# Performance work log

Hardware: AMD Instinct MI355X
Metric: run time of the kernel (lower is better)

## Reference

```python
import jax, jax.numpy as jnp
import numpy as np

B, S_ENC, S_DEC = 4, 2048, 1024
ENC_DIM, DEC_DIM, H = 1024, 1024, 16
CROSS_DIM = max(ENC_DIM, DEC_DIM)
HEAD_DIM_DEC = DEC_DIM // H
SCALE = HEAD_DIM_DEC ** 0.5  # module divides by dec_scaling only


def _linear_params(key, d_in, d_out):
    kw, kb = jax.random.split(key)
    bound = 1.0 / np.sqrt(d_in)
    W = jax.random.uniform(kw, (d_in, d_out), jnp.float32, -bound, bound)
    b = jax.random.uniform(kb, (d_out,), jnp.float32, -bound, bound)
    return W, b


def setup_inputs() -> dict:
    key = jax.random.key(0)
    ks = jax.random.split(key, 7)
    enc = jax.random.normal(ks[0], (B, S_ENC, ENC_DIM), jnp.float32)
    dec = jax.random.normal(ks[1], (B, S_DEC, DEC_DIM), jnp.float32)
    enc_mask = jax.random.uniform(ks[2], (B, 1, 1, S_ENC)) < 0.1
    q_w, q_b = _linear_params(ks[3], DEC_DIM, CROSS_DIM)
    k_w, k_b = _linear_params(ks[4], ENC_DIM, CROSS_DIM)
    v_w, v_b = _linear_params(ks[5], ENC_DIM, DEC_DIM)
    o_w, o_b = _linear_params(ks[6], DEC_DIM, DEC_DIM)
    return {"enc": enc, "enc_mask": enc_mask, "dec": dec,
            "q_w": q_w, "q_b": q_b, "k_w": k_w, "k_b": k_b,
            "v_w": v_w, "v_b": v_b, "o_w": o_w, "o_b": o_b}


def _split_heads(x):
    b, s, d = x.shape
    return x.reshape(b, s, H, d // H).transpose(0, 2, 1, 3)  # [b,h,s,hd]


def reference(enc, enc_mask, dec, q_w, q_b, k_w, k_b, v_w, v_b, o_w, o_b):
    q = _split_heads(dec @ q_w + q_b)   # [B,H,Sq,cross_hd]
    k = _split_heads(enc @ k_w + k_b)   # [B,H,Sk,cross_hd]
    v = _split_heads(enc @ v_w + v_b)   # [B,H,Sk,dec_hd]
    logits = jnp.einsum('bhqd,bhkd->bhqk', q, k) / SCALE
    logits = jnp.where(enc_mask, -jnp.inf, logits)
    a = jax.nn.softmax(logits, axis=-1)
    x = jnp.einsum('bhqk,bhkd->bhqd', a, v)          # [B,H,Sq,dec_hd]
    x = x.transpose(0, 2, 1, 3).reshape(x.shape[0], x.shape[2], -1)  # [B,Sq,DEC_DIM]
    return x @ o_w + o_b
```

## Files before the change

kernel.cpp:

```cpp
#include <hip/hip_runtime.h>
#include <hip/hip_bf16.h>
#include <cstdint>

#define BB   4
#define SENC 2048
#define SDEC 1024
#define DM   1024
#define NH   16
#define HD   64

using short8 = __attribute__((ext_vector_type(8))) short;
using f32x4  = __attribute__((ext_vector_type(4))) float;

__device__ inline unsigned short f2bf(float f) {
    return (unsigned short)((__builtin_bit_cast(unsigned int, f) + 0x8000u) >> 16);
}
__device__ inline unsigned int pk2bf(float a, float b) {
    return ((__builtin_bit_cast(unsigned int, a) + 0x8000u) >> 16) |
           ((__builtin_bit_cast(unsigned int, b) + 0x8000u) & 0xffff0000u);
}

__device__ inline float fexp2(float x) {
#if __has_builtin(__builtin_amdgcn_exp2f)
    return __builtin_amdgcn_exp2f(x);
#else
    return exp2f(x);
#endif
}

#if __has_builtin(__builtin_amdgcn_global_load_lds)
#define HAS_GLL 1
#endif

__device__ inline void stage16(const void* g, void* l) {
#ifdef HAS_GLL
    typedef __attribute__((address_space(1))) const unsigned int guint;
    typedef __attribute__((address_space(3))) unsigned int luint;
    __builtin_amdgcn_global_load_lds((guint*)g, (luint*)l, 16, 0, 0);
#else
    *(short8*)l = *(const short8*)g;
#endif
}

__global__ __launch_bounds__(256) void cvt2_kernel(const float* __restrict__ dec,
                                                   const float* __restrict__ enc,
                                                   unsigned short* __restrict__ out) {
    const int nd = BB * SDEC * DM;
    int i = (blockIdx.x * 256 + threadIdx.x) * 4;
    const float* src = (i < nd) ? (dec + i) : (enc + (i - nd));
    float4 v = *(const float4*)src;
    ushort4 o;
    o.x = f2bf(v.x); o.y = f2bf(v.y); o.z = f2bf(v.z); o.w = f2bf(v.w);
    *(ushort4*)(out + i) = o;
}

__global__ __launch_bounds__(256) void wtrans_kernel(
    const float* __restrict__ qw, const float* __restrict__ kw,
    const float* __restrict__ vw, const float* __restrict__ ow,
    unsigned short* __restrict__ qwt, unsigned short* __restrict__ kvwt,
    unsigned short* __restrict__ owt) {
    const float* src; unsigned short* dst;
    switch (blockIdx.z) {
        case 0:  src = qw; dst = qwt; break;
        case 1:  src = kw; dst = kvwt; break;
        case 2:  src = vw; dst = kvwt + (size_t)1024 * DM; break;
        default: src = ow; dst = owt; break;
    }
    __shared__ float t[64][65];
    const int k0 = blockIdx.y * 64, n0 = blockIdx.x * 64;
    const int tid = threadIdx.x;
    #pragma unroll
    for (int it = 0; it < 16; ++it) {
        int e = it * 256 + tid, r = e >> 6, c = e & 63;
        t[r][c] = src[(size_t)(k0 + r) * DM + n0 + c];
    }
    __syncthreads();
    #pragma unroll
    for (int it = 0; it < 16; ++it) {
        int e = it * 256 + tid, r = e >> 6, c = e & 63;
        dst[(size_t)(n0 + r) * DM + k0 + c] = f2bf(t[c][r]);
    }
}

__global__ __launch_bounds__(256) void gemm_qkv_kernel(
    const unsigned short* __restrict__ encb, const unsigned short* __restrict__ decb,
    const unsigned short* __restrict__ kvwt, const unsigned short* __restrict__ qwt,
    const float* __restrict__ q_b, const float* __restrict__ k_b, const float* __restrict__ v_b,
    unsigned short* __restrict__ Qb, unsigned short* __restrict__ Kb,
    unsigned short* __restrict__ Vtb) {
    __shared__ __align__(16) unsigned short As[2][128 * 32];
    __shared__ __align__(16) unsigned short Bs[2][128 * 32];
    const int id = blockIdx.x;
    const bool isKV = id < 1024;
    const unsigned short *A, *Bt;
    int m0, n0;
    if (isKV) {
        const int x = id & 7, w = id >> 3;
        A = encb; Bt = kvwt;
        m0 = (x * 8 + (w >> 4)) * 128;
        n0 = (w & 15) * 128;
    } else {
        const int i2 = id - 1024, x = i2 & 7, w = i2 >> 3;
        A = decb; Bt = qwt;
        m0 = (x * 4 + (w >> 3)) * 128;
        n0 = (w & 7) * 128;
    }
    const int tid = threadIdx.x;
    const int wave = tid >> 6, lane = tid & 63, quad = lane >> 4, l16 = lane & 15;
    const int wr = wave >> 1, wc = wave & 1;
    const int r16 = lane >> 2, c8 = (lane & 3) * 8;
    f32x4 acc[4][4] = {};

    #pragma unroll
    for (int i = 0; i < 2; ++i) {
        const int row = wave * 32 + i * 16 + r16;
        stage16(&A[(size_t)(m0 + row) * DM + c8], &As[0][row * 32 + c8]);
        stage16(&Bt[(size_t)(n0 + row) * DM + c8], &Bs[0][row * 32 + c8]);
    }
    for (int it = 0; it < 32; ++it) {
        const int bf = it & 1;
        __syncthreads();
        if (it < 31) {
            const int kb2 = (it + 1) * 32, nb = bf ^ 1;
            #pragma unroll
            for (int i = 0; i < 2; ++i) {
                const int row = wave * 32 + i * 16 + r16;
                stage16(&A[(size_t)(m0 + row) * DM + kb2 + c8], &As[nb][row * 32 + c8]);
                stage16(&Bt[(size_t)(n0 + row) * DM + kb2 + c8], &Bs[nb][row * 32 + c8]);
            }
        }
        short8 af[4], bfr[4];
        #pragma unroll
        for (int i = 0; i < 4; ++i) af[i] = *(const short8*)&As[bf][(wr * 64 + i * 16 + l16) * 32 + quad * 8];
        #pragma unroll
        for (int j = 0; j < 4; ++j) bfr[j] = *(const short8*)&Bs[bf][(wc * 64 + j * 16 + l16) * 32 + quad * 8];
        #pragma unroll
        for (int i = 0; i < 4; ++i)
            #pragma unroll
            for (int j = 0; j < 4; ++j)
                acc[i][j] = __builtin_amdgcn_mfma_f32_16x16x32_bf16(af[i], bfr[j], acc[i][j], 0, 0, 0);
    }
    #pragma unroll
    for (int i = 0; i < 4; ++i) {
        #pragma unroll
        for (int j = 0; j < 4; ++j) {
            const int gc = n0 + wc * 64 + j * 16 + l16;
            const int gr0 = m0 + wr * 64 + i * 16 + quad * 4;
            if (!isKV) {
                const float bv = q_b[gc];
                int h = gc >> 6, d = gc & 63;
                #pragma unroll
                for (int rr = 0; rr < 4; ++rr) {
                    int gr = gr0 + rr, b = gr >> 10, sq = gr & 1023;
                    float v = (acc[i][j][rr] + bv) * 0.18033688011112042f;
                    Qb[(((size_t)(b * NH + h) * SDEC + sq) << 6) + d] = f2bf(v);
                }
            } else if (gc < 1024) {
                const float bv = k_b[gc];
                int h = gc >> 6, d = gc & 63;
                #pragma unroll
                for (int rr = 0; rr < 4; ++rr) {
                    int gr = gr0 + rr, b = gr >> 11, sk = gr & 2047;
                    Kb[(((size_t)(b * NH + h) * SENC + sk) << 6) + d] = f2bf(acc[i][j][rr] + bv);
                }
            } else {
                const int gc2 = gc & 1023;
                const float bv = v_b[gc2];
                int h = gc2 >> 6, d = gc2 & 63;
                int b = gr0 >> 11, sk = gr0 & 2047;
                uint2 pk;
                pk.x = pk2bf(acc[i][j][0] + bv, acc[i][j][1] + bv);
                pk.y = pk2bf(acc[i][j][2] + bv, acc[i][j][3] + bv);
                *(uint2*)&Vtb[((size_t)(b * NH + h) * HD + d) * SENC + sk] = pk;
            }
        }
    }
}

__global__ __launch_bounds__(256) void gemm_o_kernel(const unsigned short* __restrict__ A,
                                                     const unsigned short* __restrict__ Bt,
                                                     const float* __restrict__ bias,
                                                     float* __restrict__ Cout) {
    __shared__ __align__(16) unsigned short As[2][64 * 32];
    __shared__ __align__(16) unsigned short Bs[2][128 * 32];
    const int tid = threadIdx.x;
    const int wave = tid >> 6, lane = tid & 63, quad = lane >> 4, l16 = lane & 15;
    const int m0 = blockIdx.y * 64, n0 = blockIdx.x * 128;
    const int r16 = lane >> 2, c8 = (lane & 3) * 8;
    f32x4 acc[4][2] = {};
    {
        const int rowA = wave * 16 + r16;
        stage16(&A[(size_t)(m0 + rowA) * DM + c8], &As[0][rowA * 32 + c8]);
        #pragma unroll
        for (int i = 0; i < 2; ++i) {
            const int row = wave * 32 + i * 16 + r16;
            stage16(&Bt[(size_t)(n0 + row) * DM + c8], &Bs[0][row * 32 + c8]);
        }
    }
    for (int it = 0; it < 32; ++it) {
        const int bf = it & 1;
        __syncthreads();
        if (it < 31) {
            const int kb2 = (it + 1) * 32, nb = bf ^ 1;
            const int rowA = wave * 16 + r16;
            stage16(&A[(size_t)(m0 + rowA) * DM + kb2 + c8], &As[nb][rowA * 32 + c8]);
            #pragma unroll
            for (int i = 0; i < 2; ++i) {
                const int row = wave * 32 + i * 16 + r16;
                stage16(&Bt[(size_t)(n0 + row) * DM + kb2 + c8], &Bs[nb][row * 32 + c8]);
            }
        }
        short8 af[4], bfr[2];
        #pragma unroll
        for (int i = 0; i < 4; ++i) af[i] = *(const short8*)&As[bf][(i * 16 + l16) * 32 + quad * 8];
        #pragma unroll
        for (int j = 0; j < 2; ++j) bfr[j] = *(const short8*)&Bs[bf][(wave * 32 + j * 16 + l16) * 32 + quad * 8];
        #pragma unroll
        for (int i = 0; i < 4; ++i)
            #pragma unroll
            for (int j = 0; j < 2; ++j)
                acc[i][j] = __builtin_amdgcn_mfma_f32_16x16x32_bf16(af[i], bfr[j], acc[i][j], 0, 0, 0);
    }
    #pragma unroll
    for (int i = 0; i < 4; ++i)
        #pragma unroll
        for (int j = 0; j < 2; ++j) {
            const int gc = n0 + wave * 32 + j * 16 + l16;
            const float bv = bias[gc];
            #pragma unroll
            for (int rr = 0; rr < 4; ++rr) {
                const int gr = m0 + i * 16 + quad * 4 + rr;
                Cout[(size_t)gr * DM + gc] = acc[i][j][rr] + bv;
            }
        }
}

__global__ __launch_bounds__(256, 2) void attn_kernel(const unsigned short* __restrict__ Qb,
                                                      const unsigned short* __restrict__ Kb,
                                                      const unsigned short* __restrict__ Vtb,
                                                      const int* __restrict__ mask,
                                                      unsigned short* __restrict__ Xb) {
    __shared__ __align__(16) unsigned short Ks[2][2][64 * 32];
    __shared__ __align__(16) unsigned short Vs[2][2][64 * 32];
    __shared__ __align__(16) unsigned short Ps[4][16 * 72];
    const int bh = blockIdx.y, b = bh >> 4, h = bh & 15;
    const int q0 = blockIdx.x * 128;
    const int tid = threadIdx.x, wave = tid >> 6, lane = tid & 63;
    const int quad = lane >> 4, l16 = lane & 15;
    const int sr = lane >> 2, sc = (lane & 3) * 8;

    const unsigned short* Kp = Kb + (size_t)bh * SENC * HD;
    const unsigned short* Vp = Vtb + (size_t)bh * HD * SENC;
    const int* mp = mask + (size_t)b * SENC;

    short8 qf[2][2];
    {
        const unsigned short* Qp = Qb + ((size_t)bh * SDEC + q0 + wave * 32) * HD;
        #pragma unroll
        for (int g = 0; g < 2; ++g) {
            qf[g][0] = *(const short8*)&Qp[(g * 16 + l16) * HD + quad * 8];
            qf[g][1] = *(const short8*)&Qp[(g * 16 + l16) * HD + 32 + quad * 8];
        }
    }

    float lsum[2] = {0.f, 0.f};
    f32x4 o[2][4] = {};

    {
        const unsigned short* kg = Kp + (size_t)(wave * 16 + sr) * HD;
        stage16(kg + sc,      &Ks[0][0][(wave * 16 + sr) * 32 + sc]);
        stage16(kg + 32 + sc, &Ks[0][1][(wave * 16 + sr) * 32 + sc]);
        const unsigned short* vg = Vp + (size_t)(wave * 16 + sr) * SENC;
        stage16(vg + sc,      &Vs[0][0][(wave * 16 + sr) * 32 + sc]);
        stage16(vg + 32 + sc, &Vs[0][1][(wave * 16 + sr) * 32 + sc]);
    }

    for (int it = 0; it < SENC / 64; ++it) {
        const int bf = it & 1;
        __syncthreads();
        if (it + 1 < SENC / 64) {
            const int nb = bf ^ 1, kb2 = (it + 1) * 64;
            const unsigned short* kg = Kp + (size_t)(kb2 + wave * 16 + sr) * HD;
            stage16(kg + sc,      &Ks[nb][0][(wave * 16 + sr) * 32 + sc]);
            stage16(kg + 32 + sc, &Ks[nb][1][(wave * 16 + sr) * 32 + sc]);
            const unsigned short* vg = Vp + (size_t)(wave * 16 + sr) * SENC + kb2;
            stage16(vg + sc,      &Vs[nb][0][(wave * 16 + sr) * 32 + sc]);
            stage16(vg + 32 + sc, &Vs[nb][1][(wave * 16 + sr) * 32 + sc]);
        }
        const int kb = it * 64;
        short8 kA0[4], kA1[4], vB0[4], vB1[4];
        #pragma unroll
        for (int j = 0; j < 4; ++j) {
            kA0[j] = *(const short8*)&Ks[bf][0][(j * 16 + l16) * 32 + quad * 8];
            kA1[j] = *(const short8*)&Ks[bf][1][(j * 16 + l16) * 32 + quad * 8];
            vB0[j] = *(const short8*)&Vs[bf][0][(j * 16 + l16) * 32 + quad * 8];
            vB1[j] = *(const short8*)&Vs[bf][1][(j * 16 + l16) * 32 + quad * 8];
        }
        int4 mi[4];
        #pragma unroll
        for (int j = 0; j < 4; ++j) mi[j] = *(const int4*)&mp[kb + j * 16 + quad * 4];
        #pragma unroll
        for (int g = 0; g < 2; ++g) {
            f32x4 st[4];
            #pragma unroll
            for (int j = 0; j < 4; ++j) {
                f32x4 z = {0.f, 0.f, 0.f, 0.f};
                z = __builtin_amdgcn_mfma_f32_16x16x32_bf16(kA0[j], qf[g][0], z, 0, 0, 0);
                st[j] = __builtin_amdgcn_mfma_f32_16x16x32_bf16(kA1[j], qf[g][1], z, 0, 0, 0);
            }
            #pragma unroll
            for (int j = 0; j < 4; ++j) {
                float p0 = mi[j].x ? 0.f : fexp2(st[j][0]);
                float p1 = mi[j].y ? 0.f : fexp2(st[j][1]);
                float p2 = mi[j].z ? 0.f : fexp2(st[j][2]);
                float p3 = mi[j].w ? 0.f : fexp2(st[j][3]);
                lsum[g] += (p0 + p1) + (p2 + p3);
                uint2 pkv;
                pkv.x = pk2bf(p0, p1);
                pkv.y = pk2bf(p2, p3);
                *(uint2*)&Ps[wave][l16 * 72 + j * 16 + quad * 4] = pkv;
            }
            asm volatile("s_waitcnt lgkmcnt(0)" ::: "memory");
            short8 pA0 = *(const short8*)&Ps[wave][l16 * 72 + quad * 8];
            short8 pA1 = *(const short8*)&Ps[wave][l16 * 72 + 32 + quad * 8];
            #pragma unroll
            for (int dj = 0; dj < 4; ++dj) {
                o[g][dj] = __builtin_amdgcn_mfma_f32_16x16x32_bf16(pA0, vB0[dj], o[g][dj], 0, 0, 0);
                o[g][dj] = __builtin_amdgcn_mfma_f32_16x16x32_bf16(pA1, vB1[dj], o[g][dj], 0, 0, 0);
            }
        }
    }
    #pragma unroll
    for (int g = 0; g < 2; ++g) {
        float lg = lsum[g];
        lg += __shfl_xor(lg, 16);
        lg += __shfl_xor(lg, 32);
        #pragma unroll
        for (int rr = 0; rr < 4; ++rr) {
            float iv = 1.0f / __shfl(lg, quad * 4 + rr, 64);
            int sq = q0 + wave * 32 + g * 16 + quad * 4 + rr;
            #pragma unroll
            for (int dj = 0; dj < 4; ++dj)
                Xb[((size_t)(b * SDEC) + sq) * DM + h * HD + dj * 16 + l16] = f2bf(o[g][dj][rr] * iv);
        }
    }
}

extern "C" void kernel_launch(void* const* d_in, const int* in_sizes, int n_in,
                              void* d_out, int out_size, void* d_ws, size_t ws_size,
                              hipStream_t stream) {
    const float* enc   = (const float*)d_in[0];
    const int*   emask = (const int*)d_in[1];
    const float* dec   = (const float*)d_in[2];
    const float* q_w   = (const float*)d_in[3];
    const float* q_b   = (const float*)d_in[4];
    const float* k_w   = (const float*)d_in[5];
    const float* k_b   = (const float*)d_in[6];
    const float* v_w   = (const float*)d_in[7];
    const float* v_b   = (const float*)d_in[8];
    const float* o_w   = (const float*)d_in[9];
    const float* o_b   = (const float*)d_in[10];
    float* out = (float*)d_out;

    char* ws = (char*)d_ws;
    unsigned short* decb = (unsigned short*)ws; ws += (size_t)4096 * 1024 * 2;
    unsigned short* encb = (unsigned short*)ws; ws += (size_t)8192 * 1024 * 2;
    unsigned short* qwt  = (unsigned short*)ws; ws += (size_t)1024 * 1024 * 2;
    unsigned short* kvwt = (unsigned short*)ws; ws += (size_t)2048 * 1024 * 2;
    unsigned short* owt  = (unsigned short*)ws; ws += (size_t)1024 * 1024 * 2;
    unsigned short* Qb   = (unsigned short*)ws; ws += (size_t)BB * NH * SDEC * HD * 2;
    unsigned short* Kb   = (unsigned short*)ws; ws += (size_t)BB * NH * SENC * HD * 2;
    unsigned short* Vtb  = (unsigned short*)ws; ws += (size_t)BB * NH * HD * SENC * 2;
    unsigned short* Xb   = (unsigned short*)ws; ws += (size_t)4096 * 1024 * 2;

    cvt2_kernel<<<12288, 256, 0, stream>>>(dec, enc, decb);
    wtrans_kernel<<<dim3(16, 16, 4), 256, 0, stream>>>(q_w, k_w, v_w, o_w, qwt, kvwt, owt);
    gemm_qkv_kernel<<<1280, 256, 0, stream>>>(encb, decb, kvwt, qwt, q_b, k_b, v_b, Qb, Kb, Vtb);
    attn_kernel<<<dim3(8, 64), 256, 0, stream>>>(Qb, Kb, Vtb, emask, Xb);
    gemm_o_kernel<<<dim3(8, 64), 256, 0, stream>>>(Xb, owt, o_b, out);
}
```

Baseline: 275.9 us.

## Pre-swizzle weights and K/V into MFMA fragment layout, load directly to registers

Weights, K and V^T are written in a tiled layout that matches MFMA fragment order, so each lane can read its B/K/V operand with one 16-byte global load instead of staging through LDS. This drops the K/V LDS buffers and __syncthreads in attention, and the B-operand LDS buffers in both GEMMs, using register prefetch in their place. The conversion and transpose kernels are merged into one launch, and block indices are remapped for XCD/L2 locality. The cost is heavier reliance on L2/global bandwidth, since each wave reloads shared tiles rather than reading them once into LDS. The attention launch bound also drops its 2-blocks-per-CU hint.

```diff
diff --git a/kernel.cpp b/kernel.cpp
--- a/kernel.cpp
+++ b/kernel.cpp
@@ -42,33 +42,35 @@
 #endif
 }
 
-__global__ __launch_bounds__(256) void cvt2_kernel(const float* __restrict__ dec,
-                                                   const float* __restrict__ enc,
-                                                   unsigned short* __restrict__ out) {
-    const int nd = BB * SDEC * DM;
-    int i = (blockIdx.x * 256 + threadIdx.x) * 4;
-    const float* src = (i < nd) ? (dec + i) : (enc + (i - nd));
-    float4 v = *(const float4*)src;
-    ushort4 o;
-    o.x = f2bf(v.x); o.y = f2bf(v.y); o.z = f2bf(v.z); o.w = f2bf(v.w);
-    *(ushort4*)(out + i) = o;
-}
-
-__global__ __launch_bounds__(256) void wtrans_kernel(
+__global__ __launch_bounds__(256) void prep_kernel(
+    const float* __restrict__ dec, const float* __restrict__ enc,
+    unsigned short* __restrict__ actb,
     const float* __restrict__ qw, const float* __restrict__ kw,
     const float* __restrict__ vw, const float* __restrict__ ow,
     unsigned short* __restrict__ qwt, unsigned short* __restrict__ kvwt,
     unsigned short* __restrict__ owt) {
+    __shared__ float t[64][65];
+    const int id = blockIdx.x, tid = threadIdx.x;
+    if (id < 12288) {
+        const int nd = BB * SDEC * DM;
+        int i = (id * 256 + tid) * 4;
+        const float* src = (i < nd) ? (dec + i) : (enc + (i - nd));
+        float4 v = *(const float4*)src;
+        ushort4 o;
+        o.x = f2bf(v.x); o.y = f2bf(v.y); o.z = f2bf(v.z); o.w = f2bf(v.w);
+        *(ushort4*)(actb + i) = o;
+        return;
+    }
+    const int id2 = id - 12288;
+    const int z = id2 >> 8, ky = (id2 >> 4) & 15, nx = id2 & 15;
     const float* src; unsigned short* dst;
-    switch (blockIdx.z) {
+    switch (z) {
         case 0:  src = qw; dst = qwt; break;
         case 1:  src = kw; dst = kvwt; break;
-        case 2:  src = vw; dst = kvwt + (size_t)1024 * DM; break;
+        case 2:  src = vw; dst = kvwt + (size_t)64 * 16384; break;
         default: src = ow; dst = owt; break;
     }
-    __shared__ float t[64][65];
-    const int k0 = blockIdx.y * 64, n0 = blockIdx.x * 64;
-    const int tid = threadIdx.x;
+    const int k0 = ky * 64, n0 = nx * 64;
     #pragma unroll
     for (int it = 0; it < 16; ++it) {
         int e = it * 256 + tid, r = e >> 6, c = e & 63;
@@ -78,7 +80,9 @@
     #pragma unroll
     for (int it = 0; it < 16; ++it) {
         int e = it * 256 + tid, r = e >> 6, c = e & 63;
-        dst[(size_t)(n0 + r) * DM + k0 + c] = f2bf(t[c][r]);
+        size_t off = (size_t)((n0 + r) >> 4) * 16384 + (size_t)((k0 + c) >> 3) * 128
+                   + ((r & 15) << 3) + (c & 7);
+        dst[off] = f2bf(t[c][r]);
     }
 }
 
@@ -89,19 +93,18 @@
     unsigned short* __restrict__ Qb, unsigned short* __restrict__ Kb,
     unsigned short* __restrict__ Vtb) {
     __shared__ __align__(16) unsigned short As[2][128 * 32];
-    __shared__ __align__(16) unsigned short Bs[2][128 * 32];
     const int id = blockIdx.x;
     const bool isKV = id < 1024;
-    const unsigned short *A, *Bt;
+    const unsigned short *A, *Bw;
     int m0, n0;
     if (isKV) {
         const int x = id & 7, w = id >> 3;
-        A = encb; Bt = kvwt;
+        A = encb; Bw = kvwt;
         m0 = (x * 8 + (w >> 4)) * 128;
         n0 = (w & 15) * 128;
     } else {
         const int i2 = id - 1024, x = i2 & 7, w = i2 >> 3;
-        A = decb; Bt = qwt;
+        A = decb; Bw = qwt;
         m0 = (x * 4 + (w >> 3)) * 128;
         n0 = (w & 7) * 128;
     }
@@ -111,11 +114,16 @@
     const int r16 = lane >> 2, c8 = (lane & 3) * 8;
     f32x4 acc[4][4] = {};
 
+    const unsigned short* Bbase = Bw + (size_t)(n0 >> 4) * 16384 + (size_t)(wc * 4) * 16384
+                                + quad * 128 + l16 * 8;
+    short8 bcur[4], bnxt[4];
+    #pragma unroll
+    for (int j = 0; j < 4; ++j) bcur[j] = *(const short8*)&Bbase[j * 16384];
+
     #pragma unroll
     for (int i = 0; i < 2; ++i) {
         const int row = wave * 32 + i * 16 + r16;
         stage16(&A[(size_t)(m0 + row) * DM + c8], &As[0][row * 32 + c8]);
-        stage16(&Bt[(size_t)(n0 + row) * DM + c8], &Bs[0][row * 32 + c8]);
     }
     for (int it = 0; it < 32; ++it) {
         const int bf = it & 1;
@@ -126,19 +134,21 @@
             for (int i = 0; i < 2; ++i) {
                 const int row = wave * 32 + i * 16 + r16;
                 stage16(&A[(size_t)(m0 + row) * DM + kb2 + c8], &As[nb][row * 32 + c8]);
-                stage16(&Bt[(size_t)(n0 + row) * DM + kb2 + c8], &Bs[nb][row * 32 + c8]);
-            }
-        }
-        short8 af[4], bfr[4];
+            }
+            #pragma unroll
+            for (int j = 0; j < 4; ++j)
+                bnxt[j] = *(const short8*)&Bbase[j * 16384 + kb2 * 16];
+        }
+        short8 af[4];
         #pragma unroll
         for (int i = 0; i < 4; ++i) af[i] = *(const short8*)&As[bf][(wr * 64 + i * 16 + l16) * 32 + quad * 8];
         #pragma unroll
-        for (int j = 0; j < 4; ++j) bfr[j] = *(const short8*)&Bs[bf][(wc * 64 + j * 16 + l16) * 32 + quad * 8];
-        #pragma unroll
         for (int i = 0; i < 4; ++i)
             #pragma unroll
             for (int j = 0; j < 4; ++j)
-                acc[i][j] = __builtin_amdgcn_mfma_f32_16x16x32_bf16(af[i], bfr[j], acc[i][j], 0, 0, 0);
+                acc[i][j] = __builtin_amdgcn_mfma_f32_16x16x32_bf16(af[i], bcur[j], acc[i][j], 0, 0, 0);
+        #pragma unroll
+        for (int j = 0; j < 4; ++j) bcur[j] = bnxt[j];
     }
     #pragma unroll
     for (int i = 0; i < 4; ++i) {
@@ -148,7 +158,7 @@
             const int gr0 = m0 + wr * 64 + i * 16 + quad * 4;
             if (!isKV) {
                 const float bv = q_b[gc];
-                int h = gc >> 6, d = gc & 63;
+                const int h = gc >> 6, d = gc & 63;
                 #pragma unroll
                 for (int rr = 0; rr < 4; ++rr) {
                     int gr = gr0 + rr, b = gr >> 10, sq = gr & 1023;
@@ -157,45 +167,48 @@
                 }
             } else if (gc < 1024) {
                 const float bv = k_b[gc];
-                int h = gc >> 6, d = gc & 63;
+                const int h = gc >> 6, d = gc & 63;
                 #pragma unroll
                 for (int rr = 0; rr < 4; ++rr) {
                     int gr = gr0 + rr, b = gr >> 11, sk = gr & 2047;
-                    Kb[(((size_t)(b * NH + h) * SENC + sk) << 6) + d] = f2bf(acc[i][j][rr] + bv);
+                    size_t off = (size_t)(b * NH + h) * 131072 + (size_t)(sk >> 4) * 1024
+                               + ((d >> 3) << 7) + ((sk & 15) << 3) + (d & 7);
+                    Kb[off] = f2bf(acc[i][j][rr] + bv);
                 }
             } else {
                 const int gc2 = gc & 1023;
                 const float bv = v_b[gc2];
-                int h = gc2 >> 6, d = gc2 & 63;
-                int b = gr0 >> 11, sk = gr0 & 2047;
+                const int h = gc2 >> 6, d = gc2 & 63;
+                const int b = gr0 >> 11, sk0 = gr0 & 2047;
+                size_t off = (size_t)(b * NH + h) * 131072 + (size_t)(d >> 4) * 32768
+                           + (size_t)(sk0 >> 3) * 128 + ((d & 15) << 3) + (sk0 & 7);
                 uint2 pk;
                 pk.x = pk2bf(acc[i][j][0] + bv, acc[i][j][1] + bv);
                 pk.y = pk2bf(acc[i][j][2] + bv, acc[i][j][3] + bv);
-                *(uint2*)&Vtb[((size_t)(b * NH + h) * HD + d) * SENC + sk] = pk;
+                *(uint2*)&Vtb[off] = pk;
             }
         }
     }
 }
 
 __global__ __launch_bounds__(256) void gemm_o_kernel(const unsigned short* __restrict__ A,
-                                                     const unsigned short* __restrict__ Bt,
+                                                     const unsigned short* __restrict__ Bw,
                                                      const float* __restrict__ bias,
                                                      float* __restrict__ Cout) {
     __shared__ __align__(16) unsigned short As[2][64 * 32];
-    __shared__ __align__(16) unsigned short Bs[2][128 * 32];
+    const int id = blockIdx.x, x = id & 7, w = id >> 3;
+    const int m0 = (x * 8 + (w >> 3)) * 64, n0 = (w & 7) * 128;
     const int tid = threadIdx.x;
     const int wave = tid >> 6, lane = tid & 63, quad = lane >> 4, l16 = lane & 15;
-    const int m0 = blockIdx.y * 64, n0 = blockIdx.x * 128;
     const int r16 = lane >> 2, c8 = (lane & 3) * 8;
     f32x4 acc[4][2] = {};
+    const unsigned short* Bbase = Bw + (size_t)((n0 >> 4) + wave * 2) * 16384 + quad * 128 + l16 * 8;
+    short8 bcur[2], bnxt[2];
+    #pragma unroll
+    for (int j = 0; j < 2; ++j) bcur[j] = *(const short8*)&Bbase[j * 16384];
     {
         const int rowA = wave * 16 + r16;
         stage16(&A[(size_t)(m0 + rowA) * DM + c8], &As[0][rowA * 32 + c8]);
-        #pragma unroll
-        for (int i = 0; i < 2; ++i) {
-            const int row = wave * 32 + i * 16 + r16;
-            stage16(&Bt[(size_t)(n0 + row) * DM + c8], &Bs[0][row * 32 + c8]);
-        }
     }
     for (int it = 0; it < 32; ++it) {
         const int bf = it & 1;
@@ -205,21 +218,18 @@
             const int rowA = wave * 16 + r16;
             stage16(&A[(size_t)(m0 + rowA) * DM + kb2 + c8], &As[nb][rowA * 32 + c8]);
             #pragma unroll
-            for (int i = 0; i < 2; ++i) {
-                const int row = wave * 32 + i * 16 + r16;
-                stage16(&Bt[(size_t)(n0 + row) * DM + kb2 + c8], &Bs[nb][row * 32 + c8]);
-            }
-        }
-        short8 af[4], bfr[2];
+            for (int j = 0; j < 2; ++j) bnxt[j] = *(const short8*)&Bbase[j * 16384 + kb2 * 16];
+        }
+        short8 af[4];
         #pragma unroll
         for (int i = 0; i < 4; ++i) af[i] = *(const short8*)&As[bf][(i * 16 + l16) * 32 + quad * 8];
         #pragma unroll
-        for (int j = 0; j < 2; ++j) bfr[j] = *(const short8*)&Bs[bf][(wave * 32 + j * 16 + l16) * 32 + quad * 8];
-        #pragma unroll
         for (int i = 0; i < 4; ++i)
             #pragma unroll
             for (int j = 0; j < 2; ++j)
-                acc[i][j] = __builtin_amdgcn_mfma_f32_16x16x32_bf16(af[i], bfr[j], acc[i][j], 0, 0, 0);
+                acc[i][j] = __builtin_amdgcn_mfma_f32_16x16x32_bf16(af[i], bcur[j], acc[i][j], 0, 0, 0);
+        #pragma unroll
+        for (int j = 0; j < 2; ++j) bcur[j] = bnxt[j];
     }
     #pragma unroll
     for (int i = 0; i < 4; ++i)
@@ -235,22 +245,22 @@
         }
 }
 
-__global__ __launch_bounds__(256, 2) void attn_kernel(const unsigned short* __restrict__ Qb,
-                                                      const unsigned short* __restrict__ Kb,
-                                                      const unsigned short* __restrict__ Vtb,
-                                                      const int* __restrict__ mask,
-                                                      unsigned short* __restrict__ Xb) {
-    __shared__ __align__(16) unsigned short Ks[2][2][64 * 32];
-    __shared__ __align__(16) unsigned short Vs[2][2][64 * 32];
+__global__ __launch_bounds__(256) void attn_kernel(const unsigned short* __restrict__ Qb,
+                                                   const unsigned short* __restrict__ Kb,
+                                                   const unsigned short* __restrict__ Vtb,
+                                                   const int* __restrict__ mask,
+                                                   unsigned short* __restrict__ Xb) {
     __shared__ __align__(16) unsigned short Ps[4][16 * 72];
-    const int bh = blockIdx.y, b = bh >> 4, h = bh & 15;
-    const int q0 = blockIdx.x * 128;
+    const int id = blockIdx.x, x = id & 7, r = id >> 3;
+    const int bh = x * 8 + (r & 7), qt = r >> 3;
+    const int b = bh >> 4, h = bh & 15;
+    const int q0 = qt * 128;
     const int tid = threadIdx.x, wave = tid >> 6, lane = tid & 63;
     const int quad = lane >> 4, l16 = lane & 15;
-    const int sr = lane >> 2, sc = (lane & 3) * 8;
-
-    const unsigned short* Kp = Kb + (size_t)bh * SENC * HD;
-    const unsigned short* Vp = Vtb + (size_t)bh * HD * SENC;
+    const int lo = quad * 128 + l16 * 8;
+
+    const unsigned short* Kfp = Kb + (size_t)bh * 131072;
+    const unsigned short* Vfp = Vtb + (size_t)bh * 131072;
     const int* mp = mask + (size_t)b * SENC;
 
     short8 qf[2][2];
@@ -266,35 +276,16 @@
     float lsum[2] = {0.f, 0.f};
     f32x4 o[2][4] = {};
 
-    {
-        const unsigned short* kg = Kp + (size_t)(wave * 16 + sr) * HD;
-        stage16(kg + sc,      &Ks[0][0][(wave * 16 + sr) * 32 + sc]);
-        stage16(kg + 32 + sc, &Ks[0][1][(wave * 16 + sr) * 32 + sc]);
-        const unsigned short* vg = Vp + (size_t)(wave * 16 + sr) * SENC;
-        stage16(vg + sc,      &Vs[0][0][(wave * 16 + sr) * 32 + sc]);
-        stage16(vg + 32 + sc, &Vs[0][1][(wave * 16 + sr) * 32 + sc]);
-    }
-
-    for (int it = 0; it < SENC / 64; ++it) {
-        const int bf = it & 1;
-        __syncthreads();
-        if (it + 1 < SENC / 64) {
-            const int nb = bf ^ 1, kb2 = (it + 1) * 64;
-            const unsigned short* kg = Kp + (size_t)(kb2 + wave * 16 + sr) * HD;
-            stage16(kg + sc,      &Ks[nb][0][(wave * 16 + sr) * 32 + sc]);
-            stage16(kg + 32 + sc, &Ks[nb][1][(wave * 16 + sr) * 32 + sc]);
-            const unsigned short* vg = Vp + (size_t)(wave * 16 + sr) * SENC + kb2;
-            stage16(vg + sc,      &Vs[nb][0][(wave * 16 + sr) * 32 + sc]);
-            stage16(vg + 32 + sc, &Vs[nb][1][(wave * 16 + sr) * 32 + sc]);
-        }
-        const int kb = it * 64;
+    for (int kb = 0; kb < SENC; kb += 64) {
         short8 kA0[4], kA1[4], vB0[4], vB1[4];
+        const unsigned short* kt = Kfp + (size_t)(kb >> 4) * 1024 + lo;
+        const unsigned short* vt = Vfp + (size_t)(kb >> 3) * 128 + lo;
         #pragma unroll
         for (int j = 0; j < 4; ++j) {
-            kA0[j] = *(const short8*)&Ks[bf][0][(j * 16 + l16) * 32 + quad * 8];
-            kA1[j] = *(const short8*)&Ks[bf][1][(j * 16 + l16) * 32 + quad * 8];
-            vB0[j] = *(const short8*)&Vs[bf][0][(j * 16 + l16) * 32 + quad * 8];
-            vB1[j] = *(const short8*)&Vs[bf][1][(j * 16 + l16) * 32 + quad * 8];
+            kA0[j] = *(const short8*)&kt[j * 1024];
+            kA1[j] = *(const short8*)&kt[j * 1024 + 512];
+            vB0[j] = *(const short8*)&vt[j * 32768];
+            vB1[j] = *(const short8*)&vt[j * 32768 + 512];
         }
         int4 mi[4];
         #pragma unroll
@@ -373,9 +364,8 @@
     unsigned short* Vtb  = (unsigned short*)ws; ws += (size_t)BB * NH * HD * SENC * 2;
     unsigned short* Xb   = (unsigned short*)ws; ws += (size_t)4096 * 1024 * 2;
 
-    cvt2_kernel<<<12288, 256, 0, stream>>>(dec, enc, decb);
-    wtrans_kernel<<<dim3(16, 16, 4), 256, 0, stream>>>(q_w, k_w, v_w, o_w, qwt, kvwt, owt);
+    prep_kernel<<<13312, 256, 0, stream>>>(dec, enc, decb, q_w, k_w, v_w, o_w, qwt, kvwt, owt);
     gemm_qkv_kernel<<<1280, 256, 0, stream>>>(encb, decb, kvwt, qwt, q_b, k_b, v_b, Qb, Kb, Vtb);
-    attn_kernel<<<dim3(8, 64), 256, 0, stream>>>(Qb, Kb, Vtb, emask, Xb);
-    gemm_o_kernel<<<dim3(8, 64), 256, 0, stream>>>(Xb, owt, o_b, out);
-}
+    attn_kernel<<<512, 256, 0, stream>>>(Qb, Kb, Vtb, emask, Xb);
+    gemm_o_kernel<<<512, 256, 0, stream>>>(Xb, owt, o_b, out);
+}
```

After: 253.9 us. 1.09x faster.
